# Kernel tuning notes

Measured on AMD Instinct MI355X. Metric: run time of the kernel, lower is better.

The kernel has to match this reference:

```python
import jax, jax.numpy as jnp
import numpy as np


def dct_matrix(T):
    # Orthonormal DCT-II matrix: y = D @ x  (torch_dct.dct(..., norm='ortho'))
    n = jnp.arange(T, dtype=jnp.float32)
    k = jnp.arange(T, dtype=jnp.float32)[:, None]
    D = jnp.cos(jnp.pi * (n + 0.5) * k / T) * np.sqrt(2.0 / T)
    D = D.at[0].mul(1.0 / np.sqrt(2.0))
    return D.astype(jnp.float32)


def setup_inputs() -> dict:
    key = jax.random.key(0)
    k1, k2, k3 = jax.random.split(key, 3)
    B, C, T, H, W = 8, 64, 16, 64, 64
    text_dim = 768
    r = jax.random.normal(k1, (B, C, T, H, W), dtype=jnp.float32)
    E_txt = jax.random.normal(k2, (B, text_dim), dtype=jnp.float32)
    Wf = jax.random.normal(k3, (C * T, text_dim), dtype=jnp.float32) * 0.02
    bf = jnp.zeros((C * T,), dtype=jnp.float32)
    return {"r": r, "E_txt": E_txt, "Wf": Wf, "bf": bf}


def reference(r, E_txt, Wf, bf):
    B, C, T, H, W = r.shape
    D = dct_matrix(T)  # (T, T), orthonormal so IDCT = D.T
    # DCT-II along the T axis (avoids materializing permuted copies)
    r_freq = jnp.einsum('bcthw,kt->bckhw', r, D)
    # sigmoid-gated per-(B,C,T) frequency modulation
    w = jax.nn.sigmoid((E_txt @ Wf.T + bf).reshape(B, C, T, 1, 1))
    mod = r_freq * w
    # inverse DCT (DCT-III ortho) along the frequency axis back to T
    r_out = jnp.einsum('bckhw,kt->bcthw', mod, D)
    return r_out
```

## Files before the change

### kernel.cpp

```cpp
#include <hip/hip_runtime.h>
#include <math.h>


#define HW 4096
#define HW4 1024
#define TDIM 16

__global__ __launch_bounds__(256) void gate_kernel(
    const float* __restrict__ E,
    const float* __restrict__ Wf,
    const float* __restrict__ bf,
    float* __restrict__ wout)
{
    __shared__ float Es[8 * 772];
    const float4* E4 = (const float4*)E;
    for (int i = threadIdx.x; i < 1536; i += 256) {
        int row = i / 192, col = i % 192;
        ((float4*)Es)[row * 193 + col] = E4[i];
    }
    __syncthreads();

    const int ct = blockIdx.x * 32 + (threadIdx.x >> 3);
    const int b  = threadIdx.x & 7;
    const float4* wrow = (const float4*)(Wf + ct * 768);
    const float4* erow = (const float4*)(Es + b * 772);

    float4 acc = make_float4(0.f, 0.f, 0.f, 0.f);
#pragma unroll 8
    for (int j = 0; j < 192; ++j) {
        float4 a = wrow[j];
        float4 e = erow[j];
        acc.x = fmaf(a.x, e.x, acc.x);
        acc.y = fmaf(a.y, e.y, acc.y);
        acc.z = fmaf(a.z, e.z, acc.z);
        acc.w = fmaf(a.w, e.w, acc.w);
    }
    float s = (acc.x + acc.y) + (acc.z + acc.w) + bf[ct];
    wout[b * 1024 + ct] = 1.0f / (1.0f + expf(-s));
}

__global__ __launch_bounds__(256) void mod_kernel(
    const float* __restrict__ r,
    const float* __restrict__ wbuf,
    float* __restrict__ out)
{
    __shared__ float Dl[16][16];
    __shared__ float wv[16];
    __shared__ float Msh[16][17];

    const int tid   = threadIdx.x;
    const int bc    = blockIdx.x >> 2;
    const int chunk = blockIdx.x & 3;

    {
        int k = tid >> 4, n = tid & 15;
        float v = (k == 0) ? 0.25f
                           : cospif((n + 0.5f) * (float)k * (1.0f / 16.0f)) * 0.35355339059327373f;
        Dl[k][n] = v;
        if (tid < 16) wv[tid] = wbuf[bc * 16 + tid];
    }
    __syncthreads();

    {
        int i = tid >> 4, j = tid & 15;
        float s = 0.f;
#pragma unroll
        for (int k = 0; k < 16; ++k)
            s = fmaf(Dl[k][i] * wv[k], Dl[k][j], s);
        Msh[i][j] = s;
    }
    __syncthreads();

    const size_t base = (size_t)bc * (TDIM * HW);
    const float4* rp = (const float4*)(r + base);
    float4*       op = (float4*)(out + base);
    const int hw4 = chunk * 256 + tid;

    float4 x[16];
#pragma unroll
    for (int k = 0; k < 16; ++k)
        x[k] = rp[k * HW4 + hw4];

#pragma unroll
    for (int t = 0; t < 16; ++t) {
        float4 y = make_float4(0.f, 0.f, 0.f, 0.f);
#pragma unroll
        for (int k = 0; k < 16; ++k) {
            float m = Msh[t][k];
            y.x = fmaf(m, x[k].x, y.x);
            y.y = fmaf(m, x[k].y, y.y);
            y.z = fmaf(m, x[k].z, y.z);
            y.w = fmaf(m, x[k].w, y.w);
        }
        op[t * HW4 + hw4] = y;
    }
}

extern "C" void kernel_launch(void* const* d_in, const int* in_sizes, int n_in,
                              void* d_out, int out_size, void* d_ws, size_t ws_size,
                              hipStream_t stream) {
    const float* r    = (const float*)d_in[0];
    const float* E    = (const float*)d_in[1];
    const float* Wf   = (const float*)d_in[2];
    const float* bf   = (const float*)d_in[3];
    float* out = (float*)d_out;
    float* w   = (float*)d_ws;

    gate_kernel<<<32, 256, 0, stream>>>(E, Wf, bf, w);
    mod_kernel<<<2048, 256, 0, stream>>>(r, w, out);
}
```

Baseline: 259.3 us.

## Split M construction into its own kernel and use wave-per-row gate GEMV

The gate kernel now gives each wavefront one output row. It reads Wf coalesced across lanes and reduces with shuffles, where before each thread ran a serial 768-long dot product over only 32 blocks. Building the per-(b,c) 16x16 mixing matrix moves into a separate kernel that writes to the workspace. The main modulation kernel now uses 64-thread blocks over 8192 blocks and no longer recomputes M per block. The extra kernel launch and the M round trip through global memory are meant to be outweighed by better gate parallelism and a lighter mod kernel prologue.

```diff
diff --git a/kernel.cpp b/kernel.cpp
--- a/kernel.cpp
+++ b/kernel.cpp
@@ -2,9 +2,7 @@
 #include <math.h>
 
 
-#define HW 4096
 #define HW4 1024
-#define TDIM 16
 
 __global__ __launch_bounds__(256) void gate_kernel(
     const float* __restrict__ E,
@@ -12,46 +10,53 @@
     const float* __restrict__ bf,
     float* __restrict__ wout)
 {
-    __shared__ float Es[8 * 772];
+    const int wave = threadIdx.x >> 6;
+    const int lane = threadIdx.x & 63;
+    const int ct   = blockIdx.x * 4 + wave;
+
+    const float4* W4 = (const float4*)(Wf) + ct * 192;
     const float4* E4 = (const float4*)E;
-    for (int i = threadIdx.x; i < 1536; i += 256) {
-        int row = i / 192, col = i % 192;
-        ((float4*)Es)[row * 193 + col] = E4[i];
+
+    float acc[8];
+#pragma unroll
+    for (int b = 0; b < 8; ++b) acc[b] = 0.f;
+
+#pragma unroll
+    for (int j = 0; j < 3; ++j) {
+        float4 a = W4[j * 64 + lane];
+#pragma unroll
+        for (int b = 0; b < 8; ++b) {
+            float4 e = E4[b * 192 + j * 64 + lane];
+            acc[b] = fmaf(a.x, e.x, acc[b]);
+            acc[b] = fmaf(a.y, e.y, acc[b]);
+            acc[b] = fmaf(a.z, e.z, acc[b]);
+            acc[b] = fmaf(a.w, e.w, acc[b]);
+        }
     }
-    __syncthreads();
-
-    const int ct = blockIdx.x * 32 + (threadIdx.x >> 3);
-    const int b  = threadIdx.x & 7;
-    const float4* wrow = (const float4*)(Wf + ct * 768);
-    const float4* erow = (const float4*)(Es + b * 772);
-
-    float4 acc = make_float4(0.f, 0.f, 0.f, 0.f);
-#pragma unroll 8
-    for (int j = 0; j < 192; ++j) {
-        float4 a = wrow[j];
-        float4 e = erow[j];
-        acc.x = fmaf(a.x, e.x, acc.x);
-        acc.y = fmaf(a.y, e.y, acc.y);
-        acc.z = fmaf(a.z, e.z, acc.z);
-        acc.w = fmaf(a.w, e.w, acc.w);
+#pragma unroll
+    for (int off = 32; off >= 1; off >>= 1) {
+#pragma unroll
+        for (int b = 0; b < 8; ++b)
+            acc[b] += __shfl_xor(acc[b], off, 64);
     }
-    float s = (acc.x + acc.y) + (acc.z + acc.w) + bf[ct];
-    wout[b * 1024 + ct] = 1.0f / (1.0f + expf(-s));
+    const float bias = bf[ct];
+#pragma unroll
+    for (int b = 0; b < 8; ++b) {
+        if (lane == b) {
+            float s = acc[b] + bias;
+            wout[b * 1024 + ct] = 1.0f / (1.0f + expf(-s));
+        }
+    }
 }
 
-__global__ __launch_bounds__(256) void mod_kernel(
-    const float* __restrict__ r,
+__global__ __launch_bounds__(256) void buildM_kernel(
     const float* __restrict__ wbuf,
-    float* __restrict__ out)
+    float* __restrict__ Mout)
 {
     __shared__ float Dl[16][16];
     __shared__ float wv[16];
-    __shared__ float Msh[16][17];
-
-    const int tid   = threadIdx.x;
-    const int bc    = blockIdx.x >> 2;
-    const int chunk = blockIdx.x & 3;
-
+    const int tid = threadIdx.x;
+    const int bc  = blockIdx.x;
     {
         int k = tid >> 4, n = tid & 15;
         float v = (k == 0) ? 0.25f
@@ -60,52 +65,73 @@
         if (tid < 16) wv[tid] = wbuf[bc * 16 + tid];
     }
     __syncthreads();
+    int i = tid >> 4, j = tid & 15;
+    float s = 0.f;
+#pragma unroll
+    for (int k = 0; k < 16; ++k)
+        s = fmaf(Dl[k][i] * wv[k], Dl[k][j], s);
+    Mout[bc * 256 + tid] = s;
+}
 
-    {
-        int i = tid >> 4, j = tid & 15;
-        float s = 0.f;
-#pragma unroll
-        for (int k = 0; k < 16; ++k)
-            s = fmaf(Dl[k][i] * wv[k], Dl[k][j], s);
-        Msh[i][j] = s;
-    }
+__global__ __launch_bounds__(64) void mod_kernel(
+    const float* __restrict__ r,
+    const float* __restrict__ M,
+    float* __restrict__ out)
+{
+    __shared__ float4 Ms4[64];
+    const int lane  = threadIdx.x;
+    const int bc    = blockIdx.x >> 4;
+    const int chunk = blockIdx.x & 15;
+
+    Ms4[lane] = ((const float4*)(M + bc * 256))[lane];
     __syncthreads();
+    const float* Ms = (const float*)Ms4;
 
-    const size_t base = (size_t)bc * (TDIM * HW);
+    const size_t base = (size_t)bc * (16 * 4096);
     const float4* rp = (const float4*)(r + base);
     float4*       op = (float4*)(out + base);
-    const int hw4 = chunk * 256 + tid;
+    const int col = chunk * 64 + lane;
 
     float4 x[16];
 #pragma unroll
     for (int k = 0; k < 16; ++k)
-        x[k] = rp[k * HW4 + hw4];
+        x[k] = rp[k * HW4 + col];
+
+    float4 y[16];
+#pragma unroll
+    for (int t = 0; t < 16; ++t)
+        y[t] = make_float4(0.f, 0.f, 0.f, 0.f);
 
 #pragma unroll
-    for (int t = 0; t < 16; ++t) {
-        float4 y = make_float4(0.f, 0.f, 0.f, 0.f);
+    for (int k = 0; k < 16; ++k) {
+        float4 xk = x[k];
 #pragma unroll
-        for (int k = 0; k < 16; ++k) {
-            float m = Msh[t][k];
-            y.x = fmaf(m, x[k].x, y.x);
-            y.y = fmaf(m, x[k].y, y.y);
-            y.z = fmaf(m, x[k].z, y.z);
-            y.w = fmaf(m, x[k].w, y.w);
+        for (int t = 0; t < 16; ++t) {
+            float m = Ms[t * 16 + k];
+            y[t].x = fmaf(m, xk.x, y[t].x);
+            y[t].y = fmaf(m, xk.y, y[t].y);
+            y[t].z = fmaf(m, xk.z, y[t].z);
+            y[t].w = fmaf(m, xk.w, y[t].w);
         }
-        op[t * HW4 + hw4] = y;
     }
+
+#pragma unroll
+    for (int t = 0; t < 16; ++t)
+        op[t * HW4 + col] = y[t];
 }
 
 extern "C" void kernel_launch(void* const* d_in, const int* in_sizes, int n_in,
                               void* d_out, int out_size, void* d_ws, size_t ws_size,
                               hipStream_t stream) {
-    const float* r    = (const float*)d_in[0];
-    const float* E    = (const float*)d_in[1];
-    const float* Wf   = (const float*)d_in[2];
-    const float* bf   = (const float*)d_in[3];
+    const float* r  = (const float*)d_in[0];
+    const float* E  = (const float*)d_in[1];
+    const float* Wf = (const float*)d_in[2];
+    const float* bf = (const float*)d_in[3];
     float* out = (float*)d_out;
     float* w   = (float*)d_ws;
+    float* M   = (float*)d_ws + 8192;
 
-    gate_kernel<<<32, 256, 0, stream>>>(E, Wf, bf, w);
-    mod_kernel<<<2048, 256, 0, stream>>>(r, w, out);
+    gate_kernel  <<<256, 256, 0, stream>>>(E, Wf, bf, w);
+    buildM_kernel<<<512, 256, 0, stream>>>(w, M);
+    mod_kernel   <<<8192, 64, 0, stream>>>(r, M, out);
 }
```

Result: faster. 244.0 us (-5.9%).
